# Optimization experiments

Measured on AMD Instinct MI355X. Metric: run time of the kernel, lower is better.

## Reference

```python
import jax, jax.numpy as jnp
import numpy as np

B, S, IN, OUT, E, K = 4, 2048, 4096, 4096, 8, 16
POOLS = E * K  # 128 rank-one pools


def setup_inputs() -> dict:
    key = jax.random.key(0)
    k1, k2, k3, k4, k5 = jax.random.split(key, 5)
    sc = 0.02
    return {
        "hidden_states": jax.random.normal(k1, (B, S, IN), jnp.float32),
        "w0": jax.random.normal(k2, (OUT, IN), jnp.float32) * sc,   # pretrained Linear weight
        "b0": jnp.zeros((OUT,), jnp.float32),                        # pretrained Linear bias
        "wr": jax.random.normal(k3, (POOLS, IN), jnp.float32) * sc,  # Router stacked v.T
        "u": jax.random.normal(k4, (OUT, POOLS), jnp.float32) * sc,  # RankOnePools.u
        "svh": jax.random.normal(k5, (POOLS, IN), jnp.float32) * sc, # RankOnePools.svh
        "top_k": 2,
    }


def reference(hidden_states, w0, b0, wr, u, svh, top_k):
    # pretrained dense path (expert_use_diff=True)
    pretrained_out = jnp.einsum('bsi,oi->bso', hidden_states, w0) + b0

    x = hidden_states.reshape(-1, hidden_states.shape[-1])  # [N, IN]

    # Router: logits over num_experts*k rank-one pools
    logits = jnp.einsum('ni,pi->np', x, wr)                  # [N, POOLS]
    vals, idx = jax.lax.top_k(logits, top_k)                 # [N, top_k]
    vals = vals / jnp.sum(vals, axis=-1, keepdims=True)      # computed but UNUSED (matches original torch code)

    # RankOnePools: gather selected rank-one factors and combine
    svh_sel = svh[idx]                                       # [N, top_k, IN]
    dot = jnp.einsum('ni,nti->nt', x, svh_sel)               # [N, top_k]
    u_sel = u.T[idx]                                         # [N, top_k, OUT]
    expert_out = jnp.einsum('nt,nto->no', dot, u_sel)        # [N, OUT]

    out = pretrained_out + expert_out.reshape(pretrained_out.shape)
    return out
```

## Files before the change

kernel.cpp:

```cpp
#include <hip/hip_runtime.h>

#define K_DIM  4096
#define N_OUT  4096
#define N_TOK  8192
#define N_POOL 128

typedef __bf16 bf16x8 __attribute__((ext_vector_type(8)));
typedef float  f32x4  __attribute__((ext_vector_type(4)));
typedef unsigned short u16x8 __attribute__((ext_vector_type(8)));

__device__ __forceinline__ unsigned short f2bf(float f) {
    union { float f; unsigned u; } v; v.f = f;
    unsigned r = v.u + 0x7fffu + ((v.u >> 16) & 1u);
    return (unsigned short)(r >> 16);
}
__device__ __forceinline__ float bf2f(unsigned short b) {
    union { unsigned u; float f; } v; v.u = ((unsigned)b) << 16;
    return v.f;
}

__global__ __launch_bounds__(256) void k_convert_w0(const float* __restrict__ w0,
                                                    unsigned short* __restrict__ w0b) {
    size_t base = ((size_t)blockIdx.x * 256 + threadIdx.x) * 8;
    float4 a = *(const float4*)(w0 + base);
    float4 b = *(const float4*)(w0 + base + 4);
    u16x8 r;
    r[0] = f2bf(a.x); r[1] = f2bf(a.y); r[2] = f2bf(a.z); r[3] = f2bf(a.w);
    r[4] = f2bf(b.x); r[5] = f2bf(b.y); r[6] = f2bf(b.z); r[7] = f2bf(b.w);
    *(u16x8*)(w0b + base) = r;
}

__global__ __launch_bounds__(256) void k_transpose_u(const float* __restrict__ u,
                                                     float* __restrict__ uT) {
    __shared__ float t[32][65];
    const int o0 = blockIdx.x * 64, p0 = blockIdx.y * 32;
    const int tid = threadIdx.x;
#pragma unroll
    for (int it = 0; it < 8; it++) {
        int o = (tid >> 5) + it * 8;
        t[tid & 31][o] = u[(size_t)(o0 + o) * N_POOL + p0 + (tid & 31)];
    }
    __syncthreads();
#pragma unroll
    for (int it = 0; it < 8; it++) {
        int p = (tid >> 6) + it * 4;
        uT[(size_t)(p0 + p) * N_OUT + o0 + (tid & 63)] = t[p][tid & 63];
    }
}

#define RT_TOK 32
#define RT_BK  32
#define WR_LD  132

__global__ __launch_bounds__(256) void k_router(const float* __restrict__ x,
                                                const float* __restrict__ wr,
                                                const float* __restrict__ svh,
                                                unsigned short* __restrict__ xb,
                                                int* __restrict__ idxp,
                                                float* __restrict__ dotp) {
    __shared__ float x_lds[RT_TOK][RT_BK];
    __shared__ float wr_lds[RT_BK][WR_LD];
    __shared__ float logits[RT_TOK][N_POOL + 1];
    __shared__ int   sel[RT_TOK][2];

    const int tid = threadIdx.x;
    const int m0  = blockIdx.x * RT_TOK;
    const int pg  = tid & 31;
    const int tg  = tid >> 5;

    const int xtok = tid >> 3, xk = (tid & 7) * 4;

    float acc[4][4] = {};
    float4 x_pf;
    float4 wr_pf[4];

    x_pf = *(const float4*)(x + (size_t)(m0 + xtok) * K_DIM + xk);
#pragma unroll
    for (int i = 0; i < 4; i++) {
        int cc = tid + 256 * i, p = cc >> 3, kq = (cc & 7) * 4;
        wr_pf[i] = *(const float4*)(wr + (size_t)p * K_DIM + kq);
    }

    for (int t = 0; t < K_DIM / RT_BK; t++) {
        const int k0 = t * RT_BK;
        __syncthreads();
        *(float4*)&x_lds[xtok][xk] = x_pf;
        {
            ushort4 bb;
            bb.x = f2bf(x_pf.x); bb.y = f2bf(x_pf.y); bb.z = f2bf(x_pf.z); bb.w = f2bf(x_pf.w);
            *(ushort4*)(xb + (size_t)(m0 + xtok) * K_DIM + k0 + xk) = bb;
        }
#pragma unroll
        for (int i = 0; i < 4; i++) {
            int cc = tid + 256 * i, p = cc >> 3, kq = (cc & 7) * 4;
            wr_lds[kq + 0][p] = wr_pf[i].x; wr_lds[kq + 1][p] = wr_pf[i].y;
            wr_lds[kq + 2][p] = wr_pf[i].z; wr_lds[kq + 3][p] = wr_pf[i].w;
        }
        __syncthreads();
        if (t + 1 < K_DIM / RT_BK) {
            const int kn = k0 + RT_BK;
            x_pf = *(const float4*)(x + (size_t)(m0 + xtok) * K_DIM + kn + xk);
#pragma unroll
            for (int i = 0; i < 4; i++) {
                int cc = tid + 256 * i, p = cc >> 3, kq = (cc & 7) * 4;
                wr_pf[i] = *(const float4*)(wr + (size_t)p * K_DIM + kn + kq);
            }
        }
#pragma unroll
        for (int kk = 0; kk < RT_BK; kk += 4) {
            float4 xr[4];
#pragma unroll
            for (int tt = 0; tt < 4; tt++) xr[tt] = *(float4*)&x_lds[tg * 4 + tt][kk];
#pragma unroll
            for (int j = 0; j < 4; j++) {
                float4 wv = *(float4*)&wr_lds[kk + j][pg * 4];
#pragma unroll
                for (int tt = 0; tt < 4; tt++) {
                    float a = (&xr[tt].x)[j];
                    acc[tt][0] += a * wv.x; acc[tt][1] += a * wv.y;
                    acc[tt][2] += a * wv.z; acc[tt][3] += a * wv.w;
                }
            }
        }
    }

    __syncthreads();
#pragma unroll
    for (int tt = 0; tt < 4; tt++)
#pragma unroll
        for (int q = 0; q < 4; q++)
            logits[tg * 4 + tt][pg * 4 + q] = acc[tt][q];
    __syncthreads();

    if (tid < RT_TOK) {
        float v1 = -3.4e38f, v2 = -3.4e38f; int i1 = 0, i2 = 0;
        for (int p = 0; p < N_POOL; p++) {
            float v = logits[tid][p];
            if (v > v1)      { v2 = v1; i2 = i1; v1 = v; i1 = p; }
            else if (v > v2) { v2 = v;  i2 = p; }
        }
        sel[tid][0] = i1; sel[tid][1] = i2;
        idxp[(size_t)(m0 + tid) * 2 + 0] = i1;
        idxp[(size_t)(m0 + tid) * 2 + 1] = i2;
    }
    __syncthreads();

    const int wave = tid >> 6, lane = tid & 63;
    for (int s = wave; s < RT_TOK; s += 4) {
        const size_t n = (size_t)(m0 + s);
        const int e0 = sel[s][0], e1 = sel[s][1];
        float d0 = 0.f, d1 = 0.f;
#pragma unroll
        for (int it = 0; it < 8; it++) {
            const int e = (it * 64 + lane) * 8;
            u16x8 xv = *(const u16x8*)(xb + n * K_DIM + e);
            float4 s0 = *(const float4*)(svh + (size_t)e0 * K_DIM + e);
            float4 s1 = *(const float4*)(svh + (size_t)e0 * K_DIM + e + 4);
            float4 s2 = *(const float4*)(svh + (size_t)e1 * K_DIM + e);
            float4 s3 = *(const float4*)(svh + (size_t)e1 * K_DIM + e + 4);
            float x0 = bf2f(xv[0]), x1 = bf2f(xv[1]), x2 = bf2f(xv[2]), x3 = bf2f(xv[3]);
            float x4 = bf2f(xv[4]), x5 = bf2f(xv[5]), x6 = bf2f(xv[6]), x7 = bf2f(xv[7]);
            d0 += x0*s0.x + x1*s0.y + x2*s0.z + x3*s0.w + x4*s1.x + x5*s1.y + x6*s1.z + x7*s1.w;
            d1 += x0*s2.x + x1*s2.y + x2*s2.z + x3*s2.w + x4*s3.x + x5*s3.y + x6*s3.z + x7*s3.w;
        }
#pragma unroll
        for (int off = 32; off > 0; off >>= 1) {
            d0 += __shfl_down(d0, off);
            d1 += __shfl_down(d1, off);
        }
        if (lane == 0) { dotp[n * 2 + 0] = d0; dotp[n * 2 + 1] = d1; }
    }
}

__global__ __launch_bounds__(256) void k_gemm(const unsigned short* __restrict__ xb,
                                              const unsigned short* __restrict__ w0b,
                                              const float* __restrict__ b0,
                                              const float* __restrict__ uT,
                                              const int* __restrict__ idxp,
                                              const float* __restrict__ dotp,
                                              float* __restrict__ out) {
    __shared__ unsigned short Als[128 * 64];
    __shared__ unsigned short Bls[128 * 64];

    const int tid  = threadIdx.x;
    const int lane = tid & 63;
    const int wv   = tid >> 6;
    const int wm   = wv & 1, wn = wv >> 1;
    const int lrow = lane & 15, lquad = lane >> 4;
    const size_t m0 = (size_t)blockIdx.y * 128;
    const size_t n0 = (size_t)blockIdx.x * 128;

    const int srow   = tid >> 3;
    const int xchunk = (tid & 7) ^ (srow & 7);
    const unsigned short* ag = xb  + (m0 + srow) * K_DIM + xchunk * 8;
    const unsigned short* bg = w0b + (n0 + srow) * K_DIM + xchunk * 8;
    unsigned short* al = Als + tid * 8;
    unsigned short* bl = Bls + tid * 8;

    f32x4 acc[4][4] = {};

    for (int k0 = 0; k0 < K_DIM; k0 += 64) {
        __syncthreads();
#pragma unroll
        for (int i = 0; i < 4; i++) {
            __builtin_amdgcn_global_load_lds(
                (const __attribute__((address_space(1))) void*)(ag + (size_t)i * 32 * K_DIM + k0),
                (__attribute__((address_space(3))) void*)(al + i * 2048), 16, 0, 0);
            __builtin_amdgcn_global_load_lds(
                (const __attribute__((address_space(1))) void*)(bg + (size_t)i * 32 * K_DIM + k0),
                (__attribute__((address_space(3))) void*)(bl + i * 2048), 16, 0, 0);
        }
        __syncthreads();
#pragma unroll
        for (int ks = 0; ks < 2; ks++) {
            bf16x8 af[4], bfr[4];
#pragma unroll
            for (int t = 0; t < 4; t++)
                af[t] = *(const bf16x8*)&Als[(wm * 64 + t * 16 + lrow) * 64 +
                                             (((ks * 4 + lquad) ^ (lrow & 7)) * 8)];
#pragma unroll
            for (int t = 0; t < 4; t++)
                bfr[t] = *(const bf16x8*)&Bls[(wn * 64 + t * 16 + lrow) * 64 +
                                              (((ks * 4 + lquad) ^ (lrow & 7)) * 8)];
#pragma unroll
            for (int mt = 0; mt < 4; mt++)
#pragma unroll
                for (int nt = 0; nt < 4; nt++)
                    acc[mt][nt] = __builtin_amdgcn_mfma_f32_16x16x32_bf16(af[mt], bfr[nt], acc[mt][nt], 0, 0, 0);
        }
    }

#pragma unroll
    for (int mt = 0; mt < 4; mt++) {
        const size_t rb = m0 + wm * 64 + mt * 16 + lquad * 4;
#pragma unroll
        for (int r = 0; r < 4; r++) {
            const size_t gm = rb + r;
            const int e0 = idxp[gm * 2 + 0], e1 = idxp[gm * 2 + 1];
            const float dd0 = dotp[gm * 2 + 0], dd1 = dotp[gm * 2 + 1];
#pragma unroll
            for (int nt = 0; nt < 4; nt++) {
                const size_t gn = n0 + wn * 64 + nt * 16 + lrow;
                float vv = acc[mt][nt][r] + b0[gn]
                         + dd0 * uT[(size_t)e0 * N_OUT + gn] + dd1 * uT[(size_t)e1 * N_OUT + gn];
                out[gm * N_OUT + gn] = vv;
            }
        }
    }
}

extern "C" void kernel_launch(void* const* d_in, const int* in_sizes, int n_in,
                              void* d_out, int out_size, void* d_ws, size_t ws_size,
                              hipStream_t stream) {
    const float* x   = (const float*)d_in[0];
    const float* w0  = (const float*)d_in[1];
    const float* b0  = (const float*)d_in[2];
    const float* wr  = (const float*)d_in[3];
    const float* u   = (const float*)d_in[4];
    const float* svh = (const float*)d_in[5];
    float* out = (float*)d_out;

    char* ws = (char*)d_ws;
    unsigned short* xb  = (unsigned short*)ws;
    unsigned short* w0b = (unsigned short*)(ws + 67108864);
    int*   idxp = (int*)(ws + 100663296);
    float* dotp = (float*)(ws + 100663296 + 65536);
    float* uTp  = (float*)(ws + 100663296 + 131072);

    k_convert_w0<<<dim3(16777216 / (256 * 8)), dim3(256), 0, stream>>>(w0, w0b);
    k_transpose_u<<<dim3(N_OUT / 64, N_POOL / 32), dim3(256), 0, stream>>>(u, uTp);
    k_router<<<dim3(N_TOK / RT_TOK), dim3(256), 0, stream>>>(x, wr, svh, xb, idxp, dotp);
    k_gemm<<<dim3(N_OUT / 128, N_TOK / 128), dim3(256), 0, stream>>>(xb, w0b, b0, uTp, idxp, dotp, out);
}
```

Before: 722.7 us.

## Compute router logits with split-bf16 MFMA and exact fp32 recheck for near ties

Replaces the scalar fp32 router GEMM with MFMA bf16 matrix ops. Both x and wr are split into high and low bf16 parts and combined with three MFMAs to approximate fp32 accuracy. A new pre-kernel splits wr once per call, and wr tiles are loaded straight into LDS with global_load_lds. Tokens whose second- and third-best logits fall within a tolerance get their candidate pools rescored in exact fp32 to keep top-k selection correct, at the cost of extra serial work in one wave.

```diff
diff --git a/kernel.cpp b/kernel.cpp
--- a/kernel.cpp
+++ b/kernel.cpp
@@ -30,6 +30,19 @@
     *(u16x8*)(w0b + base) = r;
 }
 
+__global__ __launch_bounds__(256) void k_split_wr(const float* __restrict__ wr,
+                                                  unsigned short* __restrict__ wrh,
+                                                  unsigned short* __restrict__ wrl) {
+    size_t base = ((size_t)blockIdx.x * 256 + threadIdx.x) * 4;
+    float4 a = *(const float4*)(wr + base);
+    ushort4 h, l;
+    h.x = f2bf(a.x); h.y = f2bf(a.y); h.z = f2bf(a.z); h.w = f2bf(a.w);
+    l.x = f2bf(a.x - bf2f(h.x)); l.y = f2bf(a.y - bf2f(h.y));
+    l.z = f2bf(a.z - bf2f(h.z)); l.w = f2bf(a.w - bf2f(h.w));
+    *(ushort4*)(wrh + base) = h;
+    *(ushort4*)(wrl + base) = l;
+}
+
 __global__ __launch_bounds__(256) void k_transpose_u(const float* __restrict__ u,
                                                      float* __restrict__ uT) {
     __shared__ float t[32][65];
@@ -48,106 +61,143 @@
     }
 }
 
-#define RT_TOK 32
-#define RT_BK  32
-#define WR_LD  132
-
-__global__ __launch_bounds__(256) void k_router(const float* __restrict__ x,
+#define RTK 64
+#define TAU 0.01f
+
+__global__ __launch_bounds__(512) void k_router(const float* __restrict__ x,
                                                 const float* __restrict__ wr,
+                                                const unsigned short* __restrict__ wrh,
+                                                const unsigned short* __restrict__ wrl,
                                                 const float* __restrict__ svh,
                                                 unsigned short* __restrict__ xb,
                                                 int* __restrict__ idxp,
                                                 float* __restrict__ dotp) {
-    __shared__ float x_lds[RT_TOK][RT_BK];
-    __shared__ float wr_lds[RT_BK][WR_LD];
-    __shared__ float logits[RT_TOK][N_POOL + 1];
-    __shared__ int   sel[RT_TOK][2];
-
-    const int tid = threadIdx.x;
-    const int m0  = blockIdx.x * RT_TOK;
-    const int pg  = tid & 31;
-    const int tg  = tid >> 5;
-
-    const int xtok = tid >> 3, xk = (tid & 7) * 4;
-
-    float acc[4][4] = {};
-    float4 x_pf;
-    float4 wr_pf[4];
-
-    x_pf = *(const float4*)(x + (size_t)(m0 + xtok) * K_DIM + xk);
-#pragma unroll
-    for (int i = 0; i < 4; i++) {
-        int cc = tid + 256 * i, p = cc >> 3, kq = (cc & 7) * 4;
-        wr_pf[i] = *(const float4*)(wr + (size_t)p * K_DIM + kq);
-    }
-
-    for (int t = 0; t < K_DIM / RT_BK; t++) {
-        const int k0 = t * RT_BK;
+    __shared__ __attribute__((aligned(16))) unsigned short Ah[32 * RTK];
+    __shared__ __attribute__((aligned(16))) unsigned short Al[32 * RTK];
+    __shared__ __attribute__((aligned(16))) unsigned short Bh[N_POOL * RTK];
+    __shared__ __attribute__((aligned(16))) unsigned short Bl[N_POOL * RTK];
+    __shared__ float lg[32][N_POOL + 1];
+    __shared__ float thr2[32];
+    __shared__ int   flg[32];
+    __shared__ int   sel[32][2];
+
+    const int tid  = threadIdx.x;
+    const int lane = tid & 63;
+    const int w    = tid >> 6;
+    const int wm   = w & 1;
+    const int wn   = w >> 1;
+    const int lrow = lane & 15, lquad = lane >> 4;
+    const size_t m0 = (size_t)blockIdx.x * 32;
+
+    const int atok  = tid >> 4;
+    const int akoff = (tid & 15) * 4;
+    const int aswz  = ((((tid & 15) >> 1) ^ (atok & 7)) * 8) + (tid & 1) * 4;
+
+    const int brow = tid >> 3;
+
+    float4 x_pf = *(const float4*)(x + (m0 + atok) * K_DIM + akoff);
+
+    f32x4 acc[2] = {};
+
+    for (int k0 = 0; k0 < K_DIM; k0 += RTK) {
         __syncthreads();
-        *(float4*)&x_lds[xtok][xk] = x_pf;
         {
-            ushort4 bb;
-            bb.x = f2bf(x_pf.x); bb.y = f2bf(x_pf.y); bb.z = f2bf(x_pf.z); bb.w = f2bf(x_pf.w);
-            *(ushort4*)(xb + (size_t)(m0 + xtok) * K_DIM + k0 + xk) = bb;
-        }
-#pragma unroll
-        for (int i = 0; i < 4; i++) {
-            int cc = tid + 256 * i, p = cc >> 3, kq = (cc & 7) * 4;
-            wr_lds[kq + 0][p] = wr_pf[i].x; wr_lds[kq + 1][p] = wr_pf[i].y;
-            wr_lds[kq + 2][p] = wr_pf[i].z; wr_lds[kq + 3][p] = wr_pf[i].w;
+            ushort4 h, l;
+            h.x = f2bf(x_pf.x); h.y = f2bf(x_pf.y); h.z = f2bf(x_pf.z); h.w = f2bf(x_pf.w);
+            l.x = f2bf(x_pf.x - bf2f(h.x)); l.y = f2bf(x_pf.y - bf2f(h.y));
+            l.z = f2bf(x_pf.z - bf2f(h.z)); l.w = f2bf(x_pf.w - bf2f(h.w));
+            *(ushort4*)(xb + (m0 + atok) * K_DIM + k0 + akoff) = h;
+            *(ushort4*)(&Ah[atok * RTK + aswz]) = h;
+            *(ushort4*)(&Al[atok * RTK + aswz]) = l;
+        }
+#pragma unroll
+        for (int i = 0; i < 2; i++) {
+            const int r = brow + i * 64;
+            const int c = (tid & 7) ^ (r & 7);
+            __builtin_amdgcn_global_load_lds(
+                (const __attribute__((address_space(1))) void*)(wrh + (size_t)r * K_DIM + k0 + c * 8),
+                (__attribute__((address_space(3))) void*)(Bh + i * 4096 + tid * 8), 16, 0, 0);
+            __builtin_amdgcn_global_load_lds(
+                (const __attribute__((address_space(1))) void*)(wrl + (size_t)r * K_DIM + k0 + c * 8),
+                (__attribute__((address_space(3))) void*)(Bl + i * 4096 + tid * 8), 16, 0, 0);
         }
         __syncthreads();
-        if (t + 1 < K_DIM / RT_BK) {
-            const int kn = k0 + RT_BK;
-            x_pf = *(const float4*)(x + (size_t)(m0 + xtok) * K_DIM + kn + xk);
-#pragma unroll
-            for (int i = 0; i < 4; i++) {
-                int cc = tid + 256 * i, p = cc >> 3, kq = (cc & 7) * 4;
-                wr_pf[i] = *(const float4*)(wr + (size_t)p * K_DIM + kn + kq);
+        if (k0 + RTK < K_DIM)
+            x_pf = *(const float4*)(x + (m0 + atok) * K_DIM + k0 + RTK + akoff);
+#pragma unroll
+        for (int ks = 0; ks < 2; ks++) {
+            const int cs = ((ks * 4 + lquad) ^ (lrow & 7)) * 8;
+            bf16x8 ah = *(const bf16x8*)&Ah[(wm * 16 + lrow) * RTK + cs];
+            bf16x8 al = *(const bf16x8*)&Al[(wm * 16 + lrow) * RTK + cs];
+#pragma unroll
+            for (int nt = 0; nt < 2; nt++) {
+                bf16x8 bh = *(const bf16x8*)&Bh[(wn * 32 + nt * 16 + lrow) * RTK + cs];
+                bf16x8 bl = *(const bf16x8*)&Bl[(wn * 32 + nt * 16 + lrow) * RTK + cs];
+                acc[nt] = __builtin_amdgcn_mfma_f32_16x16x32_bf16(ah, bh, acc[nt], 0, 0, 0);
+                acc[nt] = __builtin_amdgcn_mfma_f32_16x16x32_bf16(ah, bl, acc[nt], 0, 0, 0);
+                acc[nt] = __builtin_amdgcn_mfma_f32_16x16x32_bf16(al, bh, acc[nt], 0, 0, 0);
             }
         }
-#pragma unroll
-        for (int kk = 0; kk < RT_BK; kk += 4) {
-            float4 xr[4];
-#pragma unroll
-            for (int tt = 0; tt < 4; tt++) xr[tt] = *(float4*)&x_lds[tg * 4 + tt][kk];
-#pragma unroll
-            for (int j = 0; j < 4; j++) {
-                float4 wv = *(float4*)&wr_lds[kk + j][pg * 4];
-#pragma unroll
-                for (int tt = 0; tt < 4; tt++) {
-                    float a = (&xr[tt].x)[j];
-                    acc[tt][0] += a * wv.x; acc[tt][1] += a * wv.y;
-                    acc[tt][2] += a * wv.z; acc[tt][3] += a * wv.w;
+    }
+
+#pragma unroll
+    for (int nt = 0; nt < 2; nt++)
+#pragma unroll
+        for (int r = 0; r < 4; r++)
+            lg[wm * 16 + lquad * 4 + r][wn * 32 + nt * 16 + lrow] = acc[nt][r];
+    __syncthreads();
+
+    if (tid < 32) {
+        float v1 = -3.4e38f, v2 = -3.4e38f, v3 = -3.4e38f; int i1 = 0, i2 = 0;
+        for (int p = 0; p < N_POOL; p++) {
+            float v = lg[tid][p];
+            if (v > v1)      { v3 = v2; v2 = v1; i2 = i1; v1 = v; i1 = p; }
+            else if (v > v2) { v3 = v2; v2 = v;  i2 = p; }
+            else if (v > v3) { v3 = v; }
+        }
+        sel[tid][0] = i1; sel[tid][1] = i2;
+        thr2[tid] = v2 - TAU;
+        flg[tid]  = (v2 - v3 < TAU) ? 1 : 0;
+    }
+    __syncthreads();
+
+    if (w == 0) {
+        for (int s = 0; s < 32; s++) {
+            if (!flg[s]) continue;
+            const float th = thr2[s];
+            unsigned long long c0 = __ballot(lg[s][lane] >= th);
+            unsigned long long c1 = __ballot(lg[s][64 + lane] >= th);
+            float v1 = -3.4e38f, v2 = -3.4e38f; int i1 = 0, i2 = 0;
+            const float* xr = x + (m0 + s) * K_DIM;
+            for (int half = 0; half < 2; half++) {
+                unsigned long long m = half ? c1 : c0;
+                while (m) {
+                    const int p = (half ? 64 : 0) + __ffsll(m) - 1;
+                    m &= m - 1;
+                    const float* wp = wr + (size_t)p * K_DIM;
+                    float d = 0.f;
+#pragma unroll 8
+                    for (int it = 0; it < 64; it++)
+                        d += xr[it * 64 + lane] * wp[it * 64 + lane];
+#pragma unroll
+                    for (int off = 32; off > 0; off >>= 1) d += __shfl_down(d, off);
+                    d = __shfl(d, 0);
+                    if (d > v1)      { v2 = v1; i2 = i1; v1 = d; i1 = p; }
+                    else if (d > v2) { v2 = d; i2 = p; }
                 }
             }
-        }
-    }
-
+            if (lane == 0) { sel[s][0] = i1; sel[s][1] = i2; }
+        }
+    }
     __syncthreads();
-#pragma unroll
-    for (int tt = 0; tt < 4; tt++)
-#pragma unroll
-        for (int q = 0; q < 4; q++)
-            logits[tg * 4 + tt][pg * 4 + q] = acc[tt][q];
-    __syncthreads();
-
-    if (tid < RT_TOK) {
-        float v1 = -3.4e38f, v2 = -3.4e38f; int i1 = 0, i2 = 0;
-        for (int p = 0; p < N_POOL; p++) {
-            float v = logits[tid][p];
-            if (v > v1)      { v2 = v1; i2 = i1; v1 = v; i1 = p; }
-            else if (v > v2) { v2 = v;  i2 = p; }
-        }
-        sel[tid][0] = i1; sel[tid][1] = i2;
-        idxp[(size_t)(m0 + tid) * 2 + 0] = i1;
-        idxp[(size_t)(m0 + tid) * 2 + 1] = i2;
-    }
-    __syncthreads();
-
-    const int wave = tid >> 6, lane = tid & 63;
-    for (int s = wave; s < RT_TOK; s += 4) {
-        const size_t n = (size_t)(m0 + s);
+
+    if (tid < 32) {
+        idxp[(m0 + tid) * 2 + 0] = sel[tid][0];
+        idxp[(m0 + tid) * 2 + 1] = sel[tid][1];
+    }
+
+    for (int s = w; s < 32; s += 8) {
+        const size_t n = m0 + s;
         const int e0 = sel[s][0], e1 = sel[s][1];
         float d0 = 0.f, d1 = 0.f;
 #pragma unroll
@@ -266,9 +316,12 @@
     int*   idxp = (int*)(ws + 100663296);
     float* dotp = (float*)(ws + 100663296 + 65536);
     float* uTp  = (float*)(ws + 100663296 + 131072);
+    unsigned short* wrh = (unsigned short*)(ws + 102891520);
+    unsigned short* wrl = (unsigned short*)(ws + 103940096);
 
     k_convert_w0<<<dim3(16777216 / (256 * 8)), dim3(256), 0, stream>>>(w0, w0b);
+    k_split_wr<<<dim3(N_POOL * K_DIM / (256 * 4)), dim3(256), 0, stream>>>(wr, wrh, wrl);
     k_transpose_u<<<dim3(N_OUT / 64, N_POOL / 32), dim3(256), 0, stream>>>(u, uTp);
-    k_router<<<dim3(N_TOK / RT_TOK), dim3(256), 0, stream>>>(x, wr, svh, xb, idxp, dotp);
+    k_router<<<dim3(N_TOK / 32), dim3(512), 0, stream>>>(x, wr, wrh, wrl, svh, xb, idxp, dotp);
     k_gemm<<<dim3(N_OUT / 128, N_TOK / 128), dim3(256), 0, stream>>>(xb, w0b, b0, uTp, idxp, dotp, out);
 }
```

After: 692.5 us. 4.2% less time.
